# Kernel optimization log

Hardware: AMD Instinct MI355X
Metric: run time of the kernel (lower is better)

The kernel has to match this reference:

```python
import jax, jax.numpy as jnp
import numpy as np

NUM_HEADS = 16
HEAD_DIM = 64
INPUT_DIM = 1024
EMBED_DIM = NUM_HEADS * HEAD_DIM  # 1024


def setup_inputs() -> dict:
    key = jax.random.key(0)
    ks = jax.random.split(key, 9)
    B, S = 4, 2048
    scale = 1.0 / np.sqrt(INPUT_DIM)
    return {
        "q": jax.random.normal(ks[0], (B, S, INPUT_DIM), dtype=jnp.float32),
        "k": jax.random.normal(ks[1], (B, S, INPUT_DIM), dtype=jnp.float32),
        "v": jax.random.normal(ks[2], (B, S, INPUT_DIM), dtype=jnp.float32),
        "Wq": jax.random.normal(ks[3], (INPUT_DIM, EMBED_DIM), dtype=jnp.float32) * scale,
        "bq": jax.random.normal(ks[4], (EMBED_DIM,), dtype=jnp.float32) * 0.02,
        "Wk": jax.random.normal(ks[5], (INPUT_DIM, EMBED_DIM), dtype=jnp.float32) * scale,
        "bk": jax.random.normal(ks[6], (EMBED_DIM,), dtype=jnp.float32) * 0.02,
        "Wv": jax.random.normal(ks[7], (INPUT_DIM, EMBED_DIM), dtype=jnp.float32) * scale,
        "bv": jax.random.normal(ks[8], (EMBED_DIM,), dtype=jnp.float32) * 0.02,
    }


def reference(q, k, v, Wq, bq, Wk, bk, Wv, bv):
    B, Sq, _ = q.shape
    Sk = k.shape[1]
    # QKV projections (dropout_prob=0 -> identity; ReLU on value path)
    query = (q @ Wq + bq).reshape(B, Sq, NUM_HEADS, HEAD_DIM).transpose(0, 2, 1, 3)  # [B,H,Sq,D]
    key_ = (k @ Wk + bk).reshape(B, Sk, NUM_HEADS, HEAD_DIM).transpose(0, 2, 1, 3)   # [B,H,Sk,D]
    value = jax.nn.relu(v @ Wv + bv).reshape(B, Sk, NUM_HEADS, HEAD_DIM).transpose(0, 2, 1, 3)
    scores = jnp.einsum("bhqd,bhkd->bhqk", query, key_) / np.sqrt(HEAD_DIM).astype(np.float32)
    p_attn = jax.nn.softmax(scores, axis=-1)
    x = jnp.einsum("bhqk,bhkd->bhqd", p_attn, value)  # [B,H,Sq,D]
    return x.transpose(0, 2, 1, 3).reshape(B, Sq, EMBED_DIM)
```

## Files before the change

kernel.cpp:

```cpp
#include <hip/hip_runtime.h>
#include <hip/hip_bf16.h>
#include <stdint.h>

#define BB    4
#define NH    16
#define SEQ   2048
#define DH    64
#define EMB   1024
#define KD    1024
#define MROWS 8192

typedef short  short8  __attribute__((ext_vector_type(8)));
typedef float  f32x4   __attribute__((ext_vector_type(4)));
typedef float  f32x16  __attribute__((ext_vector_type(16)));

typedef const __attribute__((address_space(1))) void* gas_t;
typedef __attribute__((address_space(3))) void*       las_t;
#define GLD16(g, l) __builtin_amdgcn_global_load_lds((gas_t)(g), (las_t)(l), 16, 0, 0)

__device__ __forceinline__ unsigned short f2bf(float f) {
    unsigned u = __float_as_uint(f);
    u += 0x7fffu + ((u >> 16) & 1u);
    return (unsigned short)(u >> 16);
}
__device__ __forceinline__ unsigned packbf(float lo, float hi) {
    union { __hip_bfloat162 h; unsigned u; } cv;
    cv.h = __float22bfloat162_rn(make_float2(lo, hi));
    return cv.u;
}

__global__ __launch_bounds__(256) void conv3_kernel(const float* __restrict__ qf,
                                                    const float* __restrict__ kf,
                                                    const float* __restrict__ vf,
                                                    unsigned short* __restrict__ dst) {
    const int p = blockIdx.z;
    const float* src = (p == 0) ? qf : (p == 1) ? kf : vf;
    unsigned short* d = dst + (size_t)p * ((size_t)MROWS * KD);
    const size_t i = ((size_t)blockIdx.x * 256 + threadIdx.x) * 8;
    float4 f0 = *(const float4*)(src + i);
    float4 f1 = *(const float4*)(src + i + 4);
    uint4 u;
    u.x = packbf(f0.x, f0.y); u.y = packbf(f0.z, f0.w);
    u.z = packbf(f1.x, f1.y); u.w = packbf(f1.z, f1.w);
    *(uint4*)(d + i) = u;
}

__global__ __launch_bounds__(256) void wt_kernel(const float* __restrict__ Wq,
                                                 const float* __restrict__ Wk,
                                                 const float* __restrict__ Wv,
                                                 unsigned short* __restrict__ Wt) {
    __shared__ float tsh[64 * 68];
    const int p = blockIdx.z;
    const float* W = (p == 0) ? Wq : (p == 1) ? Wk : Wv;
    unsigned short* dst = Wt + (size_t)p * (KD * EMB);
    const int k0 = blockIdx.x * 64, n0 = blockIdx.y * 64;
    const int t = threadIdx.x;
    {
        const int r = t >> 2, c4 = (t & 3) * 16;
        const float* g = W + (size_t)(k0 + r) * EMB + n0 + c4;
        float* row = &tsh[r * 68 + c4];
        *(float4*)(row + 0)  = *(const float4*)(g + 0);
        *(float4*)(row + 4)  = *(const float4*)(g + 4);
        *(float4*)(row + 8)  = *(const float4*)(g + 8);
        *(float4*)(row + 12) = *(const float4*)(g + 12);
    }
    __syncthreads();
    {
        const int j = t >> 2, kp = (t & 3) * 16;
        unsigned ub[8];
#pragma unroll
        for (int ii = 0; ii < 8; ++ii)
            ub[ii] = packbf(tsh[(kp + 2 * ii) * 68 + j], tsh[(kp + 2 * ii + 1) * 68 + j]);
        unsigned short* o = dst + (size_t)(n0 + j) * KD + k0 + kp;
        *(uint4*)(o + 0) = uint4{ub[0], ub[1], ub[2], ub[3]};
        *(uint4*)(o + 8) = uint4{ub[4], ub[5], ub[6], ub[7]};
    }
}

__global__ __launch_bounds__(256) void proj_kernel(
    const unsigned short* __restrict__ AbfBase, const unsigned short* __restrict__ WtBase,
    const float* __restrict__ bq, const float* __restrict__ bk, const float* __restrict__ bv,
    unsigned short* __restrict__ Qg, unsigned short* __restrict__ Kg,
    unsigned short* __restrict__ Vt)
{
    __shared__ __align__(16) unsigned short smem[17408];
    unsigned short* Ash = smem;
    unsigned short* Bsh = smem + 8192;

    const int p = blockIdx.z;
    const unsigned short* Abf = AbfBase + (size_t)p * ((size_t)MROWS * KD);
    const unsigned short* Wp  = WtBase  + (size_t)p * (KD * EMB);
    const float* bias = (p == 0) ? bq : (p == 1) ? bk : bv;
    unsigned short* dst = (p == 0) ? Qg : (p == 1) ? Kg : Vt;

    const int row0 = blockIdx.x * 128;
    const int col0 = blockIdx.y * 128;
    const int t = threadIdx.x, lane = t & 63, wv = t >> 6;
    const int ln15 = lane & 15, q4 = lane >> 4;
    const int wm = wv & 1, wn = wv >> 1;

    f32x4 acc[4][4];
#pragma unroll
    for (int i = 0; i < 4; ++i)
#pragma unroll
        for (int j = 0; j < 4; ++j)
#pragma unroll
            for (int r = 0; r < 4; ++r) acc[i][j][r] = 0.f;

    const int lr = lane >> 3, lc = (lane & 7) ^ lr;
    const unsigned short* gA = Abf + (size_t)(row0 + wv * 32 + lr) * KD + lc * 8;
    const unsigned short* gB = Wp  + (size_t)(col0 + wv * 32 + lr) * KD + lc * 8;
    unsigned short* lA = Ash + wv * 32 * 64;
    unsigned short* lB = Bsh + wv * 32 * 64;

    for (int k0 = 0; k0 < KD; k0 += 64) {
#pragma unroll
        for (int i = 0; i < 4; ++i) {
            GLD16(gA + (size_t)i * 8 * KD + k0, lA + i * 512);
            GLD16(gB + (size_t)i * 8 * KD + k0, lB + i * 512);
        }
        __syncthreads();
#pragma unroll
        for (int kk = 0; kk < 2; ++kk) {
            short8 af[4], bfr[4];
#pragma unroll
            for (int mi = 0; mi < 4; ++mi) {
                const int r = wm * 64 + mi * 16 + ln15;
                af[mi] = *(const short8*)&Ash[r * 64 + (((kk << 2) | q4) ^ (r & 7)) * 8];
            }
#pragma unroll
            for (int ni = 0; ni < 4; ++ni) {
                const int r = wn * 64 + ni * 16 + ln15;
                bfr[ni] = *(const short8*)&Bsh[r * 64 + (((kk << 2) | q4) ^ (r & 7)) * 8];
            }
#pragma unroll
            for (int mi = 0; mi < 4; ++mi)
#pragma unroll
                for (int ni = 0; ni < 4; ++ni)
                    acc[mi][ni] = __builtin_amdgcn_mfma_f32_16x16x32_bf16(
                        af[mi], bfr[ni], acc[mi][ni], 0, 0, 0);
        }
        __syncthreads();
    }

    float bvv[4];
#pragma unroll
    for (int ni = 0; ni < 4; ++ni) bvv[ni] = bias[col0 + wn * 64 + ni * 16 + ln15];
    const float scq = 0.18033688011112042f;

    unsigned short* Tsh = smem;
#pragma unroll
    for (int mi = 0; mi < 4; ++mi)
#pragma unroll
        for (int ni = 0; ni < 4; ++ni)
#pragma unroll
            for (int r = 0; r < 4; ++r) {
                const int mr = wm * 64 + mi * 16 + q4 * 4 + r;
                const int ec = wn * 64 + ni * 16 + ln15;
                float vv = acc[mi][ni][r] + bvv[ni];
                if (p == 0) vv *= scq;
                if (p == 2) vv = vv > 0.f ? vv : 0.f;
                Tsh[mr * 136 + ec] = f2bf(vv);
            }
    __syncthreads();

    if (p < 2) {
        const int mr = t >> 1, hsel = t & 1;
        const int m = row0 + mr, bi = m >> 11, s = m & 2047;
        const int hh = (col0 >> 6) + hsel;
        const unsigned short* src = &Tsh[mr * 136 + hsel * 64];
        unsigned short* o = dst + ((size_t)(bi * NH + hh) * SEQ + s) * DH;
#pragma unroll
        for (int c = 0; c < 8; ++c)
            *(uint4*)(o + 8 * c) = *(const uint4*)(src + 8 * c);
    } else {
        const int e = t >> 1, sh2 = t & 1;
        const int n = col0 + e, hh = n >> 6, dd = n & 63;
        const int bi = row0 >> 11, sbase = (row0 & 2047) + sh2 * 64;
        unsigned ub[32];
#pragma unroll
        for (int i = 0; i < 32; ++i)
            ub[i] = (unsigned)Tsh[(sh2 * 64 + 2 * i) * 136 + e] |
                    ((unsigned)Tsh[(sh2 * 64 + 2 * i + 1) * 136 + e] << 16);
        unsigned short* o = dst + ((size_t)(bi * NH + hh) * DH + dd) * SEQ + sbase;
#pragma unroll
        for (int c = 0; c < 8; ++c)
            *(uint4*)(o + 8 * c) = uint4{ub[4 * c], ub[4 * c + 1], ub[4 * c + 2], ub[4 * c + 3]};
    }
}

__global__ __launch_bounds__(256) void attn_kernel(
    const unsigned short* __restrict__ Qg, const unsigned short* __restrict__ Kg,
    const unsigned short* __restrict__ Vt, float* __restrict__ out)
{
    __shared__ __align__(16) unsigned short smem[18432];

    const int qb = blockIdx.x, hh = blockIdx.y, bb = blockIdx.z;
    const int t = threadIdx.x, lane = t & 63, wv = t >> 6;
    const int ln31 = lane & 31, h2 = lane >> 5;
    const size_t bh = (size_t)(bb * NH + hh);
    const unsigned short* Qp = Qg + bh * (SEQ * DH);
    const unsigned short* Kp = Kg + bh * (SEQ * DH);
    const unsigned short* Vp = Vt + bh * (DH * SEQ);
    const int q0 = qb * 128 + wv * 32;

    short8 qf[4];
#pragma unroll
    for (int dc = 0; dc < 4; ++dc)
        qf[dc] = *(const short8*)(Qp + (size_t)(q0 + ln31) * DH + h2 * 8 + dc * 16);

    short8 ones;
#pragma unroll
    for (int i = 0; i < 8; ++i) ones[i] = (short)0x3F80;

    f32x16 accO[2], accL;
#pragma unroll
    for (int i = 0; i < 16; ++i) { accO[0][i] = 0.f; accO[1][i] = 0.f; accL[i] = 0.f; }

    const int srow = t >> 2, sp = (t & 3) * 16;
    const int prow = srow ^ (((((srow >> 2) ^ (srow >> 3)) & 1)) ? 12 : 0);
    const unsigned short* gk = Kp + (size_t)srow * DH + sp;
    const unsigned short* gv = Vp + (size_t)srow * SEQ + sp;
    const int wkoff = prow * 72 + sp;
    const int wvoff = 4608 + srow * 72 + sp;

    {
        short8 ka = *(const short8*)(gk), kb = *(const short8*)(gk + 8);
        short8 va = *(const short8*)(gv), vb = *(const short8*)(gv + 8);
        *(short8*)&smem[wkoff] = ka; *(short8*)&smem[wkoff + 8] = kb;
        *(short8*)&smem[wvoff] = va; *(short8*)&smem[wvoff + 8] = vb;
    }

    for (int it = 0; it < 32; ++it) {
        const int nxt = (it + 1) & 31;
        short8 ka = *(const short8*)(gk + (size_t)nxt * 64 * DH);
        short8 kb = *(const short8*)(gk + (size_t)nxt * 64 * DH + 8);
        short8 va = *(const short8*)(gv + nxt * 64);
        short8 vb = *(const short8*)(gv + nxt * 64 + 8);

        __syncthreads();

        const unsigned short* Ksh = smem + (it & 1) * 9216;
        const unsigned short* Vsh = Ksh + 4608;

        f32x16 st[2];
#pragma unroll
        for (int kt = 0; kt < 2; ++kt) {
#pragma unroll
            for (int i = 0; i < 16; ++i) st[kt][i] = 0.f;
#pragma unroll
            for (int dc = 0; dc < 4; ++dc) {
                short8 kf = *(const short8*)&Ksh[(kt * 32 + ln31) * 72 + h2 * 8 + dc * 16];
                st[kt] = __builtin_amdgcn_mfma_f32_32x32x16_bf16(kf, qf[dc], st[kt], 0, 0, 0);
            }
        }
#pragma unroll
        for (int kt = 0; kt < 2; ++kt)
#pragma unroll
            for (int r = 0; r < 16; ++r)
                st[kt][r] = __builtin_amdgcn_exp2f(st[kt][r]);

#pragma unroll
        for (int kt = 0; kt < 2; ++kt)
#pragma unroll
            for (int kc = 0; kc < 2; ++kc) {
                union { unsigned u[4]; short8 v; } pf;
#pragma unroll
                for (int i = 0; i < 4; ++i)
                    pf.u[i] = packbf(st[kt][8 * kc + 2 * i], st[kt][8 * kc + 2 * i + 1]);
                accL = __builtin_amdgcn_mfma_f32_32x32x16_bf16(ones, pf.v, accL, 0, 0, 0);
#pragma unroll
                for (int dt = 0; dt < 2; ++dt) {
                    short8 vf = *(const short8*)&Vsh[(dt * 32 + ln31) * 72 + kt * 32 + kc * 16 + h2 * 8];
                    accO[dt] = __builtin_amdgcn_mfma_f32_32x32x16_bf16(vf, pf.v, accO[dt], 0, 0, 0);
                }
            }

        unsigned short* wbuf = smem + ((it + 1) & 1) * 9216;
        *(short8*)&wbuf[wkoff] = ka; *(short8*)&wbuf[wkoff + 8] = kb;
        *(short8*)&wbuf[wvoff] = va; *(short8*)&wbuf[wvoff + 8] = vb;
    }

    const float inv = 1.0f / accL[0];
    float* orow = out + ((size_t)(bb * SEQ + q0 + ln31) * NH + hh) * 64;
#pragma unroll
    for (int dt = 0; dt < 2; ++dt)
#pragma unroll
        for (int g = 0; g < 4; ++g) {
            float4 w;
            w.x = accO[dt][4 * g + 0] * inv;
            w.y = accO[dt][4 * g + 1] * inv;
            w.z = accO[dt][4 * g + 2] * inv;
            w.w = accO[dt][4 * g + 3] * inv;
            *(float4*)(orow + dt * 32 + 4 * h2 + 8 * g) = w;
        }
}

extern "C" void kernel_launch(void* const* d_in, const int* in_sizes, int n_in,
                              void* d_out, int out_size, void* d_ws, size_t ws_size,
                              hipStream_t stream) {
    const float* qf = (const float*)d_in[0];
    const float* kf = (const float*)d_in[1];
    const float* vf = (const float*)d_in[2];
    const float* Wq = (const float*)d_in[3];
    const float* bq = (const float*)d_in[4];
    const float* Wk = (const float*)d_in[5];
    const float* bk = (const float*)d_in[6];
    const float* Wv = (const float*)d_in[7];
    const float* bv = (const float*)d_in[8];

    char* ws = (char*)d_ws;
    unsigned short* Wt  = (unsigned short*)ws;
    unsigned short* Qg  = (unsigned short*)(ws + 6291456);
    unsigned short* Kg  = Qg + 8388608;
    unsigned short* Vt  = Kg + 8388608;
    unsigned short* Ab  = Vt + 8388608;
    float* out = (float*)d_out;

    wt_kernel<<<dim3(16, 16, 3), 256, 0, stream>>>(Wq, Wk, Wv, Wt);
    conv3_kernel<<<dim3(4096, 1, 3), 256, 0, stream>>>(qf, kf, vf, Ab);
    proj_kernel<<<dim3(64, 8, 3), 256, 0, stream>>>(Ab, Wt, bq, bk, bv, Qg, Kg, Vt);
    attn_kernel<<<dim3(16, 16, 4), 256, 0, stream>>>(Qg, Kg, Vt, out);
}
```

Before: 314.8 us.

## Merge prep kernels, register-prefetch projection GEMM, double query tile per attention wave

Folds the weight-transpose and activation-convert kernels into one launch to cut per-launch overhead. Changes the projection GEMM from direct global-to-LDS loads with a 64-wide K step to register-prefetched, double-buffered 32-wide K tiles in padded LDS. In attention, each wave now handles two 32-row query tiles so every K/V fragment read from LDS feeds twice the MFMA work, with half as many blocks and launch bounds requesting two blocks per SM. The trade-offs are higher register pressure, fewer blocks to spread across CUs, and a projection inner loop with more iterations and barriers.

```diff
diff --git a/kernel.cpp b/kernel.cpp
--- a/kernel.cpp
+++ b/kernel.cpp
@@ -14,10 +14,6 @@
 typedef float  f32x4   __attribute__((ext_vector_type(4)));
 typedef float  f32x16  __attribute__((ext_vector_type(16)));
 
-typedef const __attribute__((address_space(1))) void* gas_t;
-typedef __attribute__((address_space(3))) void*       las_t;
-#define GLD16(g, l) __builtin_amdgcn_global_load_lds((gas_t)(g), (las_t)(l), 16, 0, 0)
-
 __device__ __forceinline__ unsigned short f2bf(float f) {
     unsigned u = __float_as_uint(f);
     u += 0x7fffu + ((u >> 16) & 1u);
@@ -29,51 +25,50 @@
     return cv.u;
 }
 
-__global__ __launch_bounds__(256) void conv3_kernel(const float* __restrict__ qf,
-                                                    const float* __restrict__ kf,
-                                                    const float* __restrict__ vf,
-                                                    unsigned short* __restrict__ dst) {
-    const int p = blockIdx.z;
-    const float* src = (p == 0) ? qf : (p == 1) ? kf : vf;
-    unsigned short* d = dst + (size_t)p * ((size_t)MROWS * KD);
-    const size_t i = ((size_t)blockIdx.x * 256 + threadIdx.x) * 8;
-    float4 f0 = *(const float4*)(src + i);
-    float4 f1 = *(const float4*)(src + i + 4);
-    uint4 u;
-    u.x = packbf(f0.x, f0.y); u.y = packbf(f0.z, f0.w);
-    u.z = packbf(f1.x, f1.y); u.w = packbf(f1.z, f1.w);
-    *(uint4*)(d + i) = u;
-}
-
-__global__ __launch_bounds__(256) void wt_kernel(const float* __restrict__ Wq,
-                                                 const float* __restrict__ Wk,
-                                                 const float* __restrict__ Wv,
-                                                 unsigned short* __restrict__ Wt) {
+__global__ __launch_bounds__(256) void prep_kernel(
+    const float* __restrict__ qf, const float* __restrict__ kf, const float* __restrict__ vf,
+    const float* __restrict__ Wq, const float* __restrict__ Wk, const float* __restrict__ Wv,
+    unsigned short* __restrict__ Ab, unsigned short* __restrict__ Wt)
+{
     __shared__ float tsh[64 * 68];
-    const int p = blockIdx.z;
-    const float* W = (p == 0) ? Wq : (p == 1) ? Wk : Wv;
-    unsigned short* dst = Wt + (size_t)p * (KD * EMB);
-    const int k0 = blockIdx.x * 64, n0 = blockIdx.y * 64;
-    const int t = threadIdx.x;
-    {
-        const int r = t >> 2, c4 = (t & 3) * 16;
-        const float* g = W + (size_t)(k0 + r) * EMB + n0 + c4;
-        float* row = &tsh[r * 68 + c4];
-        *(float4*)(row + 0)  = *(const float4*)(g + 0);
-        *(float4*)(row + 4)  = *(const float4*)(g + 4);
-        *(float4*)(row + 8)  = *(const float4*)(g + 8);
-        *(float4*)(row + 12) = *(const float4*)(g + 12);
-    }
-    __syncthreads();
-    {
-        const int j = t >> 2, kp = (t & 3) * 16;
-        unsigned ub[8];
-#pragma unroll
-        for (int ii = 0; ii < 8; ++ii)
-            ub[ii] = packbf(tsh[(kp + 2 * ii) * 68 + j], tsh[(kp + 2 * ii + 1) * 68 + j]);
-        unsigned short* o = dst + (size_t)(n0 + j) * KD + k0 + kp;
-        *(uint4*)(o + 0) = uint4{ub[0], ub[1], ub[2], ub[3]};
-        *(uint4*)(o + 8) = uint4{ub[4], ub[5], ub[6], ub[7]};
+    const int bx = blockIdx.x, t = threadIdx.x;
+    if (bx < 12288) {
+        const int p = bx >> 12;
+        const float* src = (p == 0) ? qf : (p == 1) ? kf : vf;
+        unsigned short* d = Ab + (size_t)p * ((size_t)MROWS * KD);
+        const size_t i = ((size_t)(bx & 4095) * 256 + t) * 8;
+        float4 f0 = *(const float4*)(src + i);
+        float4 f1 = *(const float4*)(src + i + 4);
+        uint4 u;
+        u.x = packbf(f0.x, f0.y); u.y = packbf(f0.z, f0.w);
+        u.z = packbf(f1.x, f1.y); u.w = packbf(f1.z, f1.w);
+        *(uint4*)(d + i) = u;
+    } else {
+        const int idx = bx - 12288;
+        const int p = idx >> 8, rem = idx & 255;
+        const float* W = (p == 0) ? Wq : (p == 1) ? Wk : Wv;
+        unsigned short* dst = Wt + (size_t)p * (KD * EMB);
+        const int k0 = (rem >> 4) * 64, n0 = (rem & 15) * 64;
+        {
+            const int r = t >> 2, c4 = (t & 3) * 16;
+            const float* g = W + (size_t)(k0 + r) * EMB + n0 + c4;
+            float* row = &tsh[r * 68 + c4];
+            *(float4*)(row + 0)  = *(const float4*)(g + 0);
+            *(float4*)(row + 4)  = *(const float4*)(g + 4);
+            *(float4*)(row + 8)  = *(const float4*)(g + 8);
+            *(float4*)(row + 12) = *(const float4*)(g + 12);
+        }
+        __syncthreads();
+        {
+            const int j = t >> 2, kp = (t & 3) * 16;
+            unsigned ub[8];
+#pragma unroll
+            for (int ii = 0; ii < 8; ++ii)
+                ub[ii] = packbf(tsh[(kp + 2 * ii) * 68 + j], tsh[(kp + 2 * ii + 1) * 68 + j]);
+            unsigned short* o = dst + (size_t)(n0 + j) * KD + k0 + kp;
+            *(uint4*)(o + 0) = uint4{ub[0], ub[1], ub[2], ub[3]};
+            *(uint4*)(o + 8) = uint4{ub[4], ub[5], ub[6], ub[7]};
+        }
     }
 }
 
@@ -83,9 +78,7 @@
     unsigned short* __restrict__ Qg, unsigned short* __restrict__ Kg,
     unsigned short* __restrict__ Vt)
 {
-    __shared__ __align__(16) unsigned short smem[17408];
-    unsigned short* Ash = smem;
-    unsigned short* Bsh = smem + 8192;
+    __shared__ __align__(16) unsigned short smem[18432];
 
     const int p = blockIdx.z;
     const unsigned short* Abf = AbfBase + (size_t)p * ((size_t)MROWS * KD);
@@ -107,40 +100,47 @@
 #pragma unroll
             for (int r = 0; r < 4; ++r) acc[i][j][r] = 0.f;
 
-    const int lr = lane >> 3, lc = (lane & 7) ^ lr;
-    const unsigned short* gA = Abf + (size_t)(row0 + wv * 32 + lr) * KD + lc * 8;
-    const unsigned short* gB = Wp  + (size_t)(col0 + wv * 32 + lr) * KD + lc * 8;
-    unsigned short* lA = Ash + wv * 32 * 64;
-    unsigned short* lB = Bsh + wv * 32 * 64;
-
-    for (int k0 = 0; k0 < KD; k0 += 64) {
-#pragma unroll
-        for (int i = 0; i < 4; ++i) {
-            GLD16(gA + (size_t)i * 8 * KD + k0, lA + i * 512);
-            GLD16(gB + (size_t)i * 8 * KD + k0, lB + i * 512);
-        }
+    const int tr = t >> 1, th = t & 1;
+    const unsigned short* gA = Abf + (size_t)(row0 + tr) * KD + th * 16;
+    const unsigned short* gB = Wp  + (size_t)(col0 + tr) * KD + th * 16;
+    const int woff = tr * 36 + th * 16;
+
+    short8 a0 = *(const short8*)(gA),     a1 = *(const short8*)(gA + 8);
+    short8 b0 = *(const short8*)(gB),     b1 = *(const short8*)(gB + 8);
+    {
+        unsigned short* wA = smem + woff;
+        unsigned short* wB = smem + 4608 + woff;
+        *(short8*)wA = a0; *(short8*)(wA + 8) = a1;
+        *(short8*)wB = b0; *(short8*)(wB + 8) = b1;
+    }
+
+    for (int it = 0; it < 32; ++it) {
+        const int nk = ((it + 1) & 31) * 32;
+        a0 = *(const short8*)(gA + nk); a1 = *(const short8*)(gA + nk + 8);
+        b0 = *(const short8*)(gB + nk); b1 = *(const short8*)(gB + nk + 8);
+
         __syncthreads();
-#pragma unroll
-        for (int kk = 0; kk < 2; ++kk) {
-            short8 af[4], bfr[4];
-#pragma unroll
-            for (int mi = 0; mi < 4; ++mi) {
-                const int r = wm * 64 + mi * 16 + ln15;
-                af[mi] = *(const short8*)&Ash[r * 64 + (((kk << 2) | q4) ^ (r & 7)) * 8];
-            }
-#pragma unroll
-            for (int ni = 0; ni < 4; ++ni) {
-                const int r = wn * 64 + ni * 16 + ln15;
-                bfr[ni] = *(const short8*)&Bsh[r * 64 + (((kk << 2) | q4) ^ (r & 7)) * 8];
-            }
-#pragma unroll
-            for (int mi = 0; mi < 4; ++mi)
-#pragma unroll
-                for (int ni = 0; ni < 4; ++ni)
-                    acc[mi][ni] = __builtin_amdgcn_mfma_f32_16x16x32_bf16(
-                        af[mi], bfr[ni], acc[mi][ni], 0, 0, 0);
-        }
-        __syncthreads();
+
+        const unsigned short* Acur = smem + (it & 1) * 9216;
+        const unsigned short* Bcur = Acur + 4608;
+
+        short8 af[4], bfr[4];
+#pragma unroll
+        for (int mi = 0; mi < 4; ++mi)
+            af[mi] = *(const short8*)&Acur[(wm * 64 + mi * 16 + ln15) * 36 + q4 * 8];
+#pragma unroll
+        for (int ni = 0; ni < 4; ++ni)
+            bfr[ni] = *(const short8*)&Bcur[(wn * 64 + ni * 16 + ln15) * 36 + q4 * 8];
+#pragma unroll
+        for (int mi = 0; mi < 4; ++mi)
+#pragma unroll
+            for (int ni = 0; ni < 4; ++ni)
+                acc[mi][ni] = __builtin_amdgcn_mfma_f32_16x16x32_bf16(
+                    af[mi], bfr[ni], acc[mi][ni], 0, 0, 0);
+
+        unsigned short* wbuf = smem + ((it + 1) & 1) * 9216;
+        *(short8*)&wbuf[woff] = a0; *(short8*)&wbuf[woff + 8] = a1;
+        *(short8*)&wbuf[4608 + woff] = b0; *(short8*)&wbuf[4608 + woff + 8] = b1;
     }
 
     float bvv[4];
@@ -148,6 +148,7 @@
     for (int ni = 0; ni < 4; ++ni) bvv[ni] = bias[col0 + wn * 64 + ni * 16 + ln15];
     const float scq = 0.18033688011112042f;
 
+    __syncthreads();
     unsigned short* Tsh = smem;
 #pragma unroll
     for (int mi = 0; mi < 4; ++mi)
@@ -189,7 +190,7 @@
     }
 }
 
-__global__ __launch_bounds__(256) void attn_kernel(
+__global__ __launch_bounds__(256, 2) void attn_kernel(
     const unsigned short* __restrict__ Qg, const unsigned short* __restrict__ Kg,
     const unsigned short* __restrict__ Vt, float* __restrict__ out)
 {
@@ -202,20 +203,26 @@
     const unsigned short* Qp = Qg + bh * (SEQ * DH);
     const unsigned short* Kp = Kg + bh * (SEQ * DH);
     const unsigned short* Vp = Vt + bh * (DH * SEQ);
-    const int q0 = qb * 128 + wv * 32;
-
-    short8 qf[4];
-#pragma unroll
-    for (int dc = 0; dc < 4; ++dc)
-        qf[dc] = *(const short8*)(Qp + (size_t)(q0 + ln31) * DH + h2 * 8 + dc * 16);
+    const int q0 = qb * 256 + wv * 64;
+
+    short8 qf[2][4];
+#pragma unroll
+    for (int s = 0; s < 2; ++s)
+#pragma unroll
+        for (int dc = 0; dc < 4; ++dc)
+            qf[s][dc] = *(const short8*)(Qp + (size_t)(q0 + s * 32 + ln31) * DH + h2 * 8 + dc * 16);
 
     short8 ones;
 #pragma unroll
     for (int i = 0; i < 8; ++i) ones[i] = (short)0x3F80;
 
-    f32x16 accO[2], accL;
-#pragma unroll
-    for (int i = 0; i < 16; ++i) { accO[0][i] = 0.f; accO[1][i] = 0.f; accL[i] = 0.f; }
+    f32x16 accO[2][2], accL[2];
+#pragma unroll
+    for (int i = 0; i < 16; ++i) {
+        accO[0][0][i] = 0.f; accO[0][1][i] = 0.f;
+        accO[1][0][i] = 0.f; accO[1][1][i] = 0.f;
+        accL[0][i] = 0.f; accL[1][i] = 0.f;
+    }
 
     const int srow = t >> 2, sp = (t & 3) * 16;
     const int prow = srow ^ (((((srow >> 2) ^ (srow >> 3)) & 1)) ? 12 : 0);
@@ -243,36 +250,52 @@
         const unsigned short* Ksh = smem + (it & 1) * 9216;
         const unsigned short* Vsh = Ksh + 4608;
 
-        f32x16 st[2];
-#pragma unroll
-        for (int kt = 0; kt < 2; ++kt) {
-#pragma unroll
-            for (int i = 0; i < 16; ++i) st[kt][i] = 0.f;
-#pragma unroll
-            for (int dc = 0; dc < 4; ++dc) {
-                short8 kf = *(const short8*)&Ksh[(kt * 32 + ln31) * 72 + h2 * 8 + dc * 16];
-                st[kt] = __builtin_amdgcn_mfma_f32_32x32x16_bf16(kf, qf[dc], st[kt], 0, 0, 0);
+        short8 kfr[2][4];
+#pragma unroll
+        for (int kt = 0; kt < 2; ++kt)
+#pragma unroll
+            for (int dc = 0; dc < 4; ++dc)
+                kfr[kt][dc] = *(const short8*)&Ksh[(kt * 32 + ln31) * 72 + h2 * 8 + dc * 16];
+
+        union { unsigned u[4]; short8 v; } pf[2][2][2];
+#pragma unroll
+        for (int s = 0; s < 2; ++s) {
+            f32x16 st[2];
+#pragma unroll
+            for (int kt = 0; kt < 2; ++kt) {
+#pragma unroll
+                for (int i = 0; i < 16; ++i) st[kt][i] = 0.f;
+#pragma unroll
+                for (int dc = 0; dc < 4; ++dc)
+                    st[kt] = __builtin_amdgcn_mfma_f32_32x32x16_bf16(
+                        kfr[kt][dc], qf[s][dc], st[kt], 0, 0, 0);
             }
+#pragma unroll
+            for (int kt = 0; kt < 2; ++kt)
+#pragma unroll
+                for (int r = 0; r < 16; ++r)
+                    st[kt][r] = __builtin_amdgcn_exp2f(st[kt][r]);
+#pragma unroll
+            for (int kt = 0; kt < 2; ++kt)
+#pragma unroll
+                for (int kc = 0; kc < 2; ++kc)
+#pragma unroll
+                    for (int i = 0; i < 4; ++i)
+                        pf[s][kt][kc].u[i] =
+                            packbf(st[kt][8 * kc + 2 * i], st[kt][8 * kc + 2 * i + 1]);
         }
+
 #pragma unroll
         for (int kt = 0; kt < 2; ++kt)
 #pragma unroll
-            for (int r = 0; r < 16; ++r)
-                st[kt][r] = __builtin_amdgcn_exp2f(st[kt][r]);
-
-#pragma unroll
-        for (int kt = 0; kt < 2; ++kt)
-#pragma unroll
             for (int kc = 0; kc < 2; ++kc) {
-                union { unsigned u[4]; short8 v; } pf;
-#pragma unroll
-                for (int i = 0; i < 4; ++i)
-                    pf.u[i] = packbf(st[kt][8 * kc + 2 * i], st[kt][8 * kc + 2 * i + 1]);
-                accL = __builtin_amdgcn_mfma_f32_32x32x16_bf16(ones, pf.v, accL, 0, 0, 0);
+                accL[0] = __builtin_amdgcn_mfma_f32_32x32x16_bf16(ones, pf[0][kt][kc].v, accL[0], 0, 0, 0);
+                accL[1] = __builtin_amdgcn_mfma_f32_32x32x16_bf16(ones, pf[1][kt][kc].v, accL[1], 0, 0, 0);
 #pragma unroll
                 for (int dt = 0; dt < 2; ++dt) {
                     short8 vf = *(const short8*)&Vsh[(dt * 32 + ln31) * 72 + kt * 32 + kc * 16 + h2 * 8];
-                    accO[dt] = __builtin_amdgcn_mfma_f32_32x32x16_bf16(vf, pf.v, accO[dt], 0, 0, 0);
+                    accO[0][dt] = __builtin_amdgcn_mfma_f32_32x32x16_bf16(vf, pf[0][kt][kc].v, accO[0][dt], 0, 0, 0);
+                    accO[1][dt] = __builtin_amdgcn_mfma_f32_32x32x16_bf16(vf, pf[1][kt][kc].v, accO[1][dt], 0, 0, 0);
                 }
             }
 
@@ -281,19 +304,22 @@
         *(short8*)&wbuf[wvoff] = va; *(short8*)&wbuf[wvoff + 8] = vb;
     }
 
-    const float inv = 1.0f / accL[0];
-    float* orow = out + ((size_t)(bb * SEQ + q0 + ln31) * NH + hh) * 64;
-#pragma unroll
-    for (int dt = 0; dt < 2; ++dt)
-#pragma unroll
-        for (int g = 0; g < 4; ++g) {
-            float4 w;
-            w.x = accO[dt][4 * g + 0] * inv;
-            w.y = accO[dt][4 * g + 1] * inv;
-            w.z = accO[dt][4 * g + 2] * inv;
-            w.w = accO[dt][4 * g + 3] * inv;
-            *(float4*)(orow + dt * 32 + 4 * h2 + 8 * g) = w;
-        }
+#pragma unroll
+    for (int s = 0; s < 2; ++s) {
+        const float inv = 1.0f / accL[s][0];
+        float* orow = out + ((size_t)(bb * SEQ + q0 + s * 32 + ln31) * NH + hh) * 64;
+#pragma unroll
+        for (int dt = 0; dt < 2; ++dt)
+#pragma unroll
+            for (int g = 0; g < 4; ++g) {
+                float4 w;
+                w.x = accO[s][dt][4 * g + 0] * inv;
+                w.y = accO[s][dt][4 * g + 1] * inv;
+                w.z = accO[s][dt][4 * g + 2] * inv;
+                w.w = accO[s][dt][4 * g + 3] * inv;
+                *(float4*)(orow + dt * 32 + 4 * h2 + 8 * g) = w;
+            }
+    }
 }
 
 extern "C" void kernel_launch(void* const* d_in, const int* in_sizes, int n_in,
@@ -317,8 +343,7 @@
     unsigned short* Ab  = Vt + 8388608;
     float* out = (float*)d_out;
 
-    wt_kernel<<<dim3(16, 16, 3), 256, 0, stream>>>(Wq, Wk, Wv, Wt);
-    conv3_kernel<<<dim3(4096, 1, 3), 256, 0, stream>>>(qf, kf, vf, Ab);
+    prep_kernel<<<13056, 256, 0, stream>>>(qf, kf, vf, Wq, Wk, Wv, Ab, Wt);
     proj_kernel<<<dim3(64, 8, 3), 256, 0, stream>>>(Ab, Wt, bq, bk, bv, Qg, Kg, Vt);
-    attn_kernel<<<dim3(16, 16, 4), 256, 0, stream>>>(Qg, Kg, Vt, out);
-}
+    attn_kernel<<<dim3(8, 16, 4), 256, 0, stream>>>(Qg, Kg, Vt, out);
+}
```

New measurement: 511.0 us. 1.62x slower.
